# Optimization experiments

Hardware: AMD Instinct MI355X
Metric: run time of the kernel (lower is better)

Reference implementation:

```python
import jax, jax.numpy as jnp
import numpy as np

B, LQ, LK = 4, 2048, 2048
DIM = 1024          # intermediate_dim
H, D = 16, 64       # num_heads, head_dim
AD = H * D          # attn_dim
SCALE = 1.0 / np.sqrt(D).astype(np.float32)


def setup_inputs() -> dict:
    key = jax.random.key(0)
    ks = jax.random.split(key, 12)
    init = lambda k, shape, fan_in: jax.random.normal(k, shape, jnp.float32) / np.sqrt(fan_in).astype(np.float32)
    return {
        "x": jax.random.normal(ks[0], (B, LQ, DIM), jnp.float32),
        "embeds": jax.random.normal(ks[1], (B, LK, DIM), jnp.float32),
        "Wq": init(ks[2], (DIM, AD), DIM), "bq": jnp.zeros((AD,), jnp.float32),
        "Wk": init(ks[3], (DIM, AD), DIM), "bk": jnp.zeros((AD,), jnp.float32),
        "Wv": init(ks[4], (DIM, AD), DIM), "bv": jnp.zeros((AD,), jnp.float32),
        "Wo": init(ks[5], (AD, DIM), AD), "bo": jnp.zeros((DIM,), jnp.float32),
    }


def reference(x, embeds, Wq, bq, Wk, bk, Wv, bv, Wo, bo):
    b, lq, _ = x.shape
    lk = embeds.shape[1]
    # separate QKV projections (cross-attention: K,V from embeds)
    q = (x @ Wq + bq).reshape(b, lq, H, D)
    k = (embeds @ Wk + bk).reshape(b, lk, H, D)
    v = (embeds @ Wv + bv).reshape(b, lk, H, D)
    # scaled dot-product attention; full [b,h,lq,lk] score matrix (as in source)
    scores = jnp.einsum("bqhd,bkhd->bhqk", q, k) * SCALE
    attn = jax.nn.softmax(scores, axis=-1)  # dropout is identity at eval
    ctx = jnp.einsum("bhqk,bkhd->bqhd", attn, v).reshape(b, lq, AD)
    return ctx @ Wo + bo
```

## Files before the change

kernel.cpp:

```cpp
#include <hip/hip_runtime.h>
#include <cstdint>
#include <cstddef>

#define NB   4
#define NLQ  2048
#define NLK  2048
#define NDIM 1024
#define NH   16
#define ND   64
#define NAD  1024

typedef __attribute__((ext_vector_type(8))) short bf16x8;
typedef __attribute__((ext_vector_type(4))) short sh4;
typedef __attribute__((ext_vector_type(4))) float f32x4;
typedef __attribute__((ext_vector_type(4))) int   i32x4;

static __device__ __forceinline__ short f2bf(float f) {
    unsigned u = __builtin_bit_cast(unsigned, f);
    u += 0x7fffu + ((u >> 16) & 1u);
    return (short)(u >> 16);
}

#define GLL16(GP, LP) __builtin_amdgcn_global_load_lds( \
    (const __attribute__((address_space(1))) void*)(GP), \
    (__attribute__((address_space(3))) void*)(LP), 16, 0, 0)

__global__ void cvt2(const float* __restrict__ x, const float* __restrict__ e,
                     short* __restrict__ xo, short* __restrict__ eo) {
    const float* in = blockIdx.y ? e : x;
    short* out = blockIdx.y ? eo : xo;
    int i = (blockIdx.x * blockDim.x + threadIdx.x) * 4;
    const float4 v = *(const float4*)(in + i);
    sh4 o;
    o.x = f2bf(v.x); o.y = f2bf(v.y); o.z = f2bf(v.z); o.w = f2bf(v.w);
    *(sh4*)(out + i) = o;
}

__global__ void wtrans4(const float* __restrict__ W0, const float* __restrict__ W1,
                        const float* __restrict__ W2, const float* __restrict__ W3,
                        short* __restrict__ T0, short* __restrict__ T1,
                        short* __restrict__ T2, short* __restrict__ T3) {
    __shared__ float t[32][33];
    const int z = blockIdx.z;
    const float* W = (z == 0) ? W0 : (z == 1) ? W1 : (z == 2) ? W2 : W3;
    short* Wt = (z == 0) ? T0 : (z == 1) ? T1 : (z == 2) ? T2 : T3;
    const int bx = blockIdx.x * 32;
    const int by = blockIdx.y * 32;
    const int tx = threadIdx.x & 31, ty = threadIdx.x >> 5;
    #pragma unroll
    for (int i = 0; i < 32; i += 8)
        t[ty + i][tx] = W[(size_t)(bx + ty + i) * 1024 + by + tx];
    __syncthreads();
    #pragma unroll
    for (int i = 0; i < 32; i += 8)
        Wt[(size_t)(by + ty + i) * 1024 + bx + tx] = f2bf(t[tx][ty + i]);
}


__global__ __launch_bounds__(256) void gemm_qkv(const short* __restrict__ Xb,
                                                const short* __restrict__ Eb,
                                                const short* __restrict__ Wqt,
                                                const short* __restrict__ Wkt,
                                                const short* __restrict__ Wvt,
                                                const float* __restrict__ bq,
                                                const float* __restrict__ bk,
                                                const float* __restrict__ bv,
                                                short* __restrict__ Qb,
                                                short* __restrict__ Kf,
                                                short* __restrict__ Vtb)
{
    const int N = 1024, K = 1024;
    __shared__ __align__(16) short As[128 * 64];
    __shared__ __align__(16) short Bs[128 * 64];
    const int z = blockIdx.z;
    const short* A    = (z == 0) ? Xb : Eb;
    const short* Wt   = (z == 0) ? Wqt : (z == 1) ? Wkt : Wvt;
    const float* bias = (z == 0) ? bq : (z == 1) ? bk : bv;
    const float scale = (z == 0) ? 0.18033688011112042f : 1.0f;

    const int tid = threadIdx.x, wave = tid >> 6, lane = tid & 63;
    const int quad = lane >> 4, col = lane & 15;
    const int m0 = blockIdx.x * 128, n0 = blockIdx.y * 128;
    const int wm = wave >> 1, wn = wave & 1;

    const f32x4 zero = {0.f, 0.f, 0.f, 0.f};
    f32x4 acc[4][4];
    #pragma unroll
    for (int i = 0; i < 4; ++i)
        #pragma unroll
        for (int j = 0; j < 4; ++j)
            acc[i][j] = zero;

    for (int kt = 0; kt < K / 64; ++kt) {
        __syncthreads();
        #pragma unroll
        for (int i = 0; i < 4; ++i) {
            const int f = (i * 4 + wave) * 512 + lane * 8;
            const int row = f >> 6, ch = (f >> 3) & 7;
            const int gcol = kt * 64 + ((ch ^ (row & 7)) * 8);
            GLL16(A  + (size_t)(m0 + row) * K + gcol, &As[f]);
            GLL16(Wt + (size_t)(n0 + row) * K + gcol, &Bs[f]);
        }
        __syncthreads();
        #pragma unroll
        for (int kk = 0; kk < 2; ++kk) {
            bf16x8 af[4], bfr[4];
            #pragma unroll
            for (int mt = 0; mt < 4; ++mt) {
                const int r = wm * 64 + mt * 16 + col;
                af[mt] = *(const bf16x8*)&As[r * 64 + (((kk * 4 + quad) ^ (r & 7)) * 8)];
            }
            #pragma unroll
            for (int nt = 0; nt < 4; ++nt) {
                const int r = wn * 64 + nt * 16 + col;
                bfr[nt] = *(const bf16x8*)&Bs[r * 64 + (((kk * 4 + quad) ^ (r & 7)) * 8)];
            }
            #pragma unroll
            for (int mt = 0; mt < 4; ++mt)
                #pragma unroll
                for (int nt = 0; nt < 4; ++nt)
                    acc[mt][nt] = __builtin_amdgcn_mfma_f32_16x16x32_bf16(af[mt], bfr[nt], acc[mt][nt], 0, 0, 0);
        }
    }

    if (z < 2) {
        short* outp = (z == 0) ? Qb : Kf;
        #pragma unroll
        for (int mt = 0; mt < 4; ++mt)
            #pragma unroll
            for (int nt = 0; nt < 4; ++nt) {
                const int n = n0 + wn * 64 + nt * 16 + col;
                const float bv_ = bias[n];
                #pragma unroll
                for (int r = 0; r < 4; ++r) {
                    const int m = m0 + wm * 64 + mt * 16 + quad * 4 + r;
                    outp[(size_t)m * N + n] = f2bf((acc[mt][nt][r] + bv_) * scale);
                }
            }
    } else {
        #pragma unroll
        for (int mt = 0; mt < 4; ++mt)
            #pragma unroll
            for (int nt = 0; nt < 4; ++nt) {
                const int n = n0 + wn * 64 + nt * 16 + col;
                const int hh = n >> 6, d = n & 63;
                const float bv_ = bias[n];
                const int mb = m0 + wm * 64 + mt * 16 + quad * 4;
                const int bb = mb >> 11, s = mb & 2047;
                sh4 o4;
                #pragma unroll
                for (int r = 0; r < 4; ++r)
                    o4[r] = f2bf(acc[mt][nt][r] + bv_);
                *(sh4*)&Vtb[((size_t)((bb * NH + hh) * 64 + d)) * NLK + s] = o4;
            }
    }
}

__global__ __launch_bounds__(256) void gemm_out(const short* __restrict__ A,
                                                const short* __restrict__ Wt,
                                                const float* __restrict__ bias,
                                                float* __restrict__ outp)
{
    const int N = 1024, K = 1024;
    __shared__ __align__(16) short As[128 * 64];
    __shared__ __align__(16) short Bs[128 * 64];
    const int tid = threadIdx.x, wave = tid >> 6, lane = tid & 63;
    const int quad = lane >> 4, col = lane & 15;
    const int m0 = blockIdx.x * 128, n0 = blockIdx.y * 128;
    const int wm = wave >> 1, wn = wave & 1;

    const f32x4 zero = {0.f, 0.f, 0.f, 0.f};
    f32x4 acc[4][4];
    #pragma unroll
    for (int i = 0; i < 4; ++i)
        #pragma unroll
        for (int j = 0; j < 4; ++j)
            acc[i][j] = zero;

    for (int kt = 0; kt < K / 64; ++kt) {
        __syncthreads();
        #pragma unroll
        for (int i = 0; i < 4; ++i) {
            const int f = (i * 4 + wave) * 512 + lane * 8;
            const int row = f >> 6, ch = (f >> 3) & 7;
            const int gcol = kt * 64 + ((ch ^ (row & 7)) * 8);
            GLL16(A  + (size_t)(m0 + row) * K + gcol, &As[f]);
            GLL16(Wt + (size_t)(n0 + row) * K + gcol, &Bs[f]);
        }
        __syncthreads();
        #pragma unroll
        for (int kk = 0; kk < 2; ++kk) {
            bf16x8 af[4], bfr[4];
            #pragma unroll
            for (int mt = 0; mt < 4; ++mt) {
                const int r = wm * 64 + mt * 16 + col;
                af[mt] = *(const bf16x8*)&As[r * 64 + (((kk * 4 + quad) ^ (r & 7)) * 8)];
            }
            #pragma unroll
            for (int nt = 0; nt < 4; ++nt) {
                const int r = wn * 64 + nt * 16 + col;
                bfr[nt] = *(const bf16x8*)&Bs[r * 64 + (((kk * 4 + quad) ^ (r & 7)) * 8)];
            }
            #pragma unroll
            for (int mt = 0; mt < 4; ++mt)
                #pragma unroll
                for (int nt = 0; nt < 4; ++nt)
                    acc[mt][nt] = __builtin_amdgcn_mfma_f32_16x16x32_bf16(af[mt], bfr[nt], acc[mt][nt], 0, 0, 0);
        }
    }

    #pragma unroll
    for (int mt = 0; mt < 4; ++mt)
        #pragma unroll
        for (int nt = 0; nt < 4; ++nt) {
            const int n = n0 + wn * 64 + nt * 16 + col;
            const float bv_ = bias[n];
            #pragma unroll
            for (int r = 0; r < 4; ++r) {
                const int m = m0 + wm * 64 + mt * 16 + quad * 4 + r;
                outp[(size_t)m * N + n] = acc[mt][nt][r] + bv_;
            }
        }
}

__global__ __launch_bounds__(256, 2) void attn_fused6(const short* __restrict__ Q,
                                                      const short* __restrict__ Kb,
                                                      const short* __restrict__ Vt,
                                                      short* __restrict__ ctx)
{
    __shared__ __align__(16) short Ks[64 * 64];
    __shared__ __align__(16) short Vs[64 * 64];
    const int tid = threadIdx.x, wave = tid >> 6, lane = tid & 63;
    const int quad = lane >> 4, col = lane & 15;
    const int h = blockIdx.y, b = blockIdx.z;
    const int q0 = blockIdx.x * 256 + wave * 64;

    bf16x8 aq[4][2];
    #pragma unroll
    for (int mt = 0; mt < 4; ++mt) {
        const short* qp = Q + (size_t)(b * NLQ + q0 + mt * 16 + col) * NAD + h * 64 + quad * 8;
        aq[mt][0] = *(const bf16x8*)qp;
        aq[mt][1] = *(const bf16x8*)(qp + 32);
    }

    bf16x8 vones;
    #pragma unroll
    for (int j = 0; j < 8; ++j) vones[j] = (short)0x3F80;

    const f32x4 zero = {0.f, 0.f, 0.f, 0.f};
    f32x4 O[4][4];
    f32x4 Ol[4];
    #pragma unroll
    for (int mt = 0; mt < 4; ++mt) {
        Ol[mt] = zero;
        #pragma unroll
        for (int db = 0; db < 4; ++db) O[db][mt] = zero;
    }

    const int srow = tid >> 3, schunk = tid & 7;
    const short* kbase = Kb + (size_t)b * NLK * NAD + h * 64 + schunk * 8;
    const short* vbase = Vt + (size_t)(b * NH + h) * 64 * NLK + schunk * 8;

    bf16x8 kv[2], vv[2];
    #pragma unroll
    for (int i = 0; i < 2; ++i) {
        const int row = i * 32 + srow;
        kv[i] = *(const bf16x8*)(kbase + (size_t)row * NAD);
        vv[i] = *(const bf16x8*)(vbase + (size_t)row * NLK);
    }

    for (int kt = 0; kt < NLK / 64; ++kt) {
        __syncthreads();
        #pragma unroll
        for (int i = 0; i < 2; ++i) {
            const int row = i * 32 + srow;
            const int c = (schunk ^ (row & 7)) * 8;
            *(bf16x8*)&Ks[row * 64 + c] = kv[i];
            *(bf16x8*)&Vs[row * 64 + c] = vv[i];
        }
        __syncthreads();

        const int nk = (kt + 1) & (NLK / 64 - 1);
        #pragma unroll
        for (int i = 0; i < 2; ++i) {
            const int row = i * 32 + srow;
            kv[i] = *(const bf16x8*)(kbase + (size_t)(nk * 64 + row) * NAD);
            vv[i] = *(const bf16x8*)(vbase + (size_t)row * NLK + nk * 64);
        }

        bf16x8 kf[2][4];
        #pragma unroll
        for (int kk = 0; kk < 2; ++kk)
            #pragma unroll
            for (int nt = 0; nt < 4; ++nt) {
                const int key = nt * 16 + col;
                kf[kk][nt] = *(const bf16x8*)&Ks[key * 64 + (((kk * 4 + quad) ^ (key & 7)) * 8)];
            }

        int pk[4][2][4];
        #pragma unroll
        for (int mt = 0; mt < 4; ++mt) {
            f32x4 st[4];
            #pragma unroll
            for (int nt = 0; nt < 4; ++nt) st[nt] = zero;
            #pragma unroll
            for (int kk = 0; kk < 2; ++kk)
                #pragma unroll
                for (int nt = 0; nt < 4; ++nt)
                    st[nt] = __builtin_amdgcn_mfma_f32_16x16x32_bf16(kf[kk][nt], aq[mt][kk], st[nt], 0, 0, 0);
            #pragma unroll
            for (int nt = 0; nt < 4; ++nt) {
                const unsigned u0 = __builtin_bit_cast(unsigned, __builtin_amdgcn_exp2f(st[nt][0]));
                const unsigned u1 = __builtin_bit_cast(unsigned, __builtin_amdgcn_exp2f(st[nt][1]));
                const unsigned u2 = __builtin_bit_cast(unsigned, __builtin_amdgcn_exp2f(st[nt][2]));
                const unsigned u3 = __builtin_bit_cast(unsigned, __builtin_amdgcn_exp2f(st[nt][3]));
                const int t = nt >> 1, odd = (nt & 1) * 2;
                pk[mt][t][odd + 0] = (int)__builtin_amdgcn_perm(u1, u0, 0x07060302u);
                pk[mt][t][odd + 1] = (int)__builtin_amdgcn_perm(u3, u2, 0x07060302u);
            }
            #pragma unroll
            for (int t = 0; t < 2; ++t) {
                const bf16x8 pb = __builtin_bit_cast(bf16x8,
                    i32x4{pk[mt][t][0], pk[mt][t][1], pk[mt][t][2], pk[mt][t][3]});
                Ol[mt] = __builtin_amdgcn_mfma_f32_16x16x32_bf16(vones, pb, Ol[mt], 0, 0, 0);
            }
        }

        #pragma unroll
        for (int t = 0; t < 2; ++t)
            #pragma unroll
            for (int db = 0; db < 4; ++db) {
                const int row = db * 16 + col;
                const int c0 = t * 32 + quad * 4;
                const int c1 = t * 32 + 16 + quad * 4;
                const sh4 lo = *(const sh4*)&Vs[row * 64 + (((c0 >> 3) ^ (row & 7)) * 8 + (c0 & 7))];
                const sh4 hi = *(const sh4*)&Vs[row * 64 + (((c1 >> 3) ^ (row & 7)) * 8 + (c1 & 7))];
                bf16x8 va;
                #pragma unroll
                for (int j = 0; j < 4; ++j) { va[j] = lo[j]; va[j + 4] = hi[j]; }
                #pragma unroll
                for (int mt = 0; mt < 4; ++mt) {
                    const bf16x8 pb = __builtin_bit_cast(bf16x8,
                        i32x4{pk[mt][t][0], pk[mt][t][1], pk[mt][t][2], pk[mt][t][3]});
                    O[db][mt] = __builtin_amdgcn_mfma_f32_16x16x32_bf16(va, pb, O[db][mt], 0, 0, 0);
                }
            }
    }

    #pragma unroll
    for (int mt = 0; mt < 4; ++mt) {
        const float linv = 1.0f / Ol[mt][0];
        #pragma unroll
        for (int db = 0; db < 4; ++db) {
            sh4 o4;
            #pragma unroll
            for (int r = 0; r < 4; ++r)
                o4[r] = f2bf(O[db][mt][r] * linv);
            short* cp = ctx + (size_t)(b * NLQ + q0 + mt * 16 + col) * NAD
                      + h * 64 + db * 16 + quad * 4;
            *(sh4*)cp = o4;
        }
    }
}

extern "C" void kernel_launch(void* const* d_in, const int* in_sizes, int n_in,
                              void* d_out, int out_size, void* d_ws, size_t ws_size,
                              hipStream_t stream)
{
    (void)in_sizes; (void)n_in; (void)out_size; (void)ws_size;
    const float* x  = (const float*)d_in[0];
    const float* e  = (const float*)d_in[1];
    const float* Wq = (const float*)d_in[2];
    const float* bq = (const float*)d_in[3];
    const float* Wk = (const float*)d_in[4];
    const float* bk = (const float*)d_in[5];
    const float* Wv = (const float*)d_in[6];
    const float* bv = (const float*)d_in[7];
    const float* Wo = (const float*)d_in[8];
    const float* bo = (const float*)d_in[9];
    float* out = (float*)d_out;

    const size_t MQ = (size_t)NB * NLQ;
    short* wsp = (short*)d_ws;
    short* Xb  = wsp;
    short* Eb  = Xb  + MQ * NDIM;
    short* Wqt = Eb  + MQ * NDIM;
    short* Wkt = Wqt + (size_t)NDIM * NAD;
    short* Wvt = Wkt + (size_t)NDIM * NAD;
    short* Wot = Wvt + (size_t)NDIM * NAD;
    short* Qb  = Wot + (size_t)NDIM * NAD;
    short* Kf  = Qb  + MQ * NAD;
    short* Vtb = Kf  + MQ * NAD;
    short* Cx  = Vtb + MQ * NAD;

    cvt2<<<dim3(8192, 2), 256, 0, stream>>>(x, e, Xb, Eb);
    wtrans4<<<dim3(32, 32, 4), 256, 0, stream>>>(Wq, Wk, Wv, Wo, Wqt, Wkt, Wvt, Wot);

    gemm_qkv<<<dim3(64, 8, 3), 256, 0, stream>>>(Xb, Eb, Wqt, Wkt, Wvt,
                                                 bq, bk, bv, Qb, Kf, Vtb);

    attn_fused6<<<dim3(NLQ / 256, NH, NB), 256, 0, stream>>>(Qb, Kf, Vtb, Cx);

    gemm_out<<<dim3(64, 8), 256, 0, stream>>>(Cx, Wot, bo, out);
}
```

Before: 299.6 us.

## Rewrite QKV GEMM with 256x256 tiles, double-buffered LDS and scheduled barriers

The QKV projection GEMM moves from 128x128 tiles on 256 threads with synchronous single-buffer loads to 256x256 tiles on 512 threads. Global-to-LDS loads are double-buffered, with explicit vmcnt waits, so loads overlap the MFMA work. Each wave loads its fragments into registers and then runs the MFMA burst at raised priority between explicit barriers. Larger tiles improve data reuse, but the grid shrinks to 384 blocks and the kernel uses 128KB of LDS, which limits occupancy.

```diff
diff --git a/kernel.cpp b/kernel.cpp
--- a/kernel.cpp
+++ b/kernel.cpp
@@ -24,6 +24,12 @@
 #define GLL16(GP, LP) __builtin_amdgcn_global_load_lds( \
     (const __attribute__((address_space(1))) void*)(GP), \
     (__attribute__((address_space(3))) void*)(LP), 16, 0, 0)
+
+#define SBAR do { __builtin_amdgcn_sched_barrier(0); asm volatile("" ::: "memory"); \
+                  __builtin_amdgcn_s_barrier(); \
+                  asm volatile("" ::: "memory"); __builtin_amdgcn_sched_barrier(0); } while (0)
+#define WAITVM(N) do { asm volatile("s_waitcnt vmcnt(" #N ")" ::: "memory"); \
+                       __builtin_amdgcn_sched_barrier(0); } while (0)
 
 __global__ void cvt2(const float* __restrict__ x, const float* __restrict__ e,
                      short* __restrict__ xo, short* __restrict__ eo) {
@@ -56,22 +62,20 @@
         Wt[(size_t)(by + ty + i) * 1024 + bx + tx] = f2bf(t[tx][ty + i]);
 }
 
-
-__global__ __launch_bounds__(256) void gemm_qkv(const short* __restrict__ Xb,
-                                                const short* __restrict__ Eb,
-                                                const short* __restrict__ Wqt,
-                                                const short* __restrict__ Wkt,
-                                                const short* __restrict__ Wvt,
-                                                const float* __restrict__ bq,
-                                                const float* __restrict__ bk,
-                                                const float* __restrict__ bv,
-                                                short* __restrict__ Qb,
-                                                short* __restrict__ Kf,
-                                                short* __restrict__ Vtb)
+__global__ __launch_bounds__(512, 2) void gemm_qkv2(const short* __restrict__ Xb,
+                                                    const short* __restrict__ Eb,
+                                                    const short* __restrict__ Wqt,
+                                                    const short* __restrict__ Wkt,
+                                                    const short* __restrict__ Wvt,
+                                                    const float* __restrict__ bq,
+                                                    const float* __restrict__ bk,
+                                                    const float* __restrict__ bv,
+                                                    short* __restrict__ Qb,
+                                                    short* __restrict__ Kf,
+                                                    short* __restrict__ Vtb)
 {
-    const int N = 1024, K = 1024;
-    __shared__ __align__(16) short As[128 * 64];
-    __shared__ __align__(16) short Bs[128 * 64];
+    const int NT = 16;
+    __shared__ __align__(16) short lds[2][2 * 256 * 64];
     const int z = blockIdx.z;
     const short* A    = (z == 0) ? Xb : Eb;
     const short* Wt   = (z == 0) ? Wqt : (z == 1) ? Wkt : Wvt;
@@ -80,79 +84,114 @@
 
     const int tid = threadIdx.x, wave = tid >> 6, lane = tid & 63;
     const int quad = lane >> 4, col = lane & 15;
-    const int m0 = blockIdx.x * 128, n0 = blockIdx.y * 128;
-    const int wm = wave >> 1, wn = wave & 1;
+    const int m0 = blockIdx.x * 256, n0 = blockIdx.y * 256;
+    const int wm = wave >> 2, wn = wave & 3;
 
     const f32x4 zero = {0.f, 0.f, 0.f, 0.f};
-    f32x4 acc[4][4];
-    #pragma unroll
-    for (int i = 0; i < 4; ++i)
+    f32x4 acc[8][4];
+    #pragma unroll
+    for (int i = 0; i < 8; ++i)
         #pragma unroll
         for (int j = 0; j < 4; ++j)
             acc[i][j] = zero;
 
-    for (int kt = 0; kt < K / 64; ++kt) {
-        __syncthreads();
+    auto STAGE = [&](short* buf, int t) {
         #pragma unroll
         for (int i = 0; i < 4; ++i) {
-            const int f = (i * 4 + wave) * 512 + lane * 8;
-            const int row = f >> 6, ch = (f >> 3) & 7;
-            const int gcol = kt * 64 + ((ch ^ (row & 7)) * 8);
-            GLL16(A  + (size_t)(m0 + row) * K + gcol, &As[f]);
-            GLL16(Wt + (size_t)(n0 + row) * K + gcol, &Bs[f]);
-        }
-        __syncthreads();
-        #pragma unroll
-        for (int kk = 0; kk < 2; ++kk) {
-            bf16x8 af[4], bfr[4];
-            #pragma unroll
-            for (int mt = 0; mt < 4; ++mt) {
-                const int r = wm * 64 + mt * 16 + col;
-                af[mt] = *(const bf16x8*)&As[r * 64 + (((kk * 4 + quad) ^ (r & 7)) * 8)];
-            }
-            #pragma unroll
-            for (int nt = 0; nt < 4; ++nt) {
-                const int r = wn * 64 + nt * 16 + col;
-                bfr[nt] = *(const bf16x8*)&Bs[r * 64 + (((kk * 4 + quad) ^ (r & 7)) * 8)];
-            }
-            #pragma unroll
-            for (int mt = 0; mt < 4; ++mt)
-                #pragma unroll
-                for (int nt = 0; nt < 4; ++nt)
-                    acc[mt][nt] = __builtin_amdgcn_mfma_f32_16x16x32_bf16(af[mt], bfr[nt], acc[mt][nt], 0, 0, 0);
-        }
+            const int f = (i * 8 + wave) * 64 + lane;
+            const int row = f >> 3, ch = f & 7;
+            const int gcol = t * 64 + ((ch ^ (row & 7)) * 8);
+            GLL16(A  + (size_t)(m0 + row) * 1024 + gcol, buf + f * 8);
+            GLL16(Wt + (size_t)(n0 + row) * 1024 + gcol, buf + 256 * 64 + f * 8);
+        }
+    };
+
+    auto COMPUTE = [&](const short* Abuf, const short* Bbuf) {
+        #pragma unroll
+        for (int qm = 0; qm < 2; ++qm)
+            #pragma unroll
+            for (int qn = 0; qn < 2; ++qn) {
+                bf16x8 af[2][4], bfr[2][2];
+                #pragma unroll
+                for (int kk = 0; kk < 2; ++kk) {
+                    #pragma unroll
+                    for (int mt = 0; mt < 4; ++mt) {
+                        const int r = wm * 128 + qm * 64 + mt * 16 + col;
+                        af[kk][mt] = *(const bf16x8*)&Abuf[r * 64 + (((kk * 4 + quad) ^ (r & 7)) * 8)];
+                    }
+                    #pragma unroll
+                    for (int nt = 0; nt < 2; ++nt) {
+                        const int r = wn * 64 + qn * 32 + nt * 16 + col;
+                        bfr[kk][nt] = *(const bf16x8*)&Bbuf[r * 64 + (((kk * 4 + quad) ^ (r & 7)) * 8)];
+                    }
+                }
+                SBAR;
+                __builtin_amdgcn_s_setprio(1);
+                #pragma unroll
+                for (int kk = 0; kk < 2; ++kk)
+                    #pragma unroll
+                    for (int mt = 0; mt < 4; ++mt)
+                        #pragma unroll
+                        for (int nt = 0; nt < 2; ++nt)
+                            acc[qm * 4 + mt][qn * 2 + nt] =
+                                __builtin_amdgcn_mfma_f32_16x16x32_bf16(af[kk][mt], bfr[kk][nt],
+                                                                        acc[qm * 4 + mt][qn * 2 + nt], 0, 0, 0);
+                __builtin_amdgcn_s_setprio(0);
+                SBAR;
+            }
+    };
+
+    short* L0 = &lds[0][0];
+    short* L1 = &lds[1][0];
+
+    STAGE(L0, 0);
+    STAGE(L1, 1);
+    WAITVM(8);
+    SBAR;
+
+    for (int t2 = 0; t2 < NT; t2 += 2) {
+        COMPUTE(L0, L0 + 256 * 64);
+        SBAR;
+        if (t2 + 2 < NT) { STAGE(L0, t2 + 2); WAITVM(8); }
+        else             { WAITVM(0); }
+        SBAR;
+        COMPUTE(L1, L1 + 256 * 64);
+        SBAR;
+        if (t2 + 3 < NT) { STAGE(L1, t2 + 3); WAITVM(8); }
+        SBAR;
     }
 
     if (z < 2) {
         short* outp = (z == 0) ? Qb : Kf;
         #pragma unroll
-        for (int mt = 0; mt < 4; ++mt)
+        for (int mt = 0; mt < 8; ++mt) {
+            const int mbase = m0 + wm * 128 + (mt >> 2) * 64 + (mt & 3) * 16 + quad * 4;
             #pragma unroll
             for (int nt = 0; nt < 4; ++nt) {
-                const int n = n0 + wn * 64 + nt * 16 + col;
+                const int n = n0 + wn * 64 + (nt >> 1) * 32 + (nt & 1) * 16 + col;
                 const float bv_ = bias[n];
                 #pragma unroll
-                for (int r = 0; r < 4; ++r) {
-                    const int m = m0 + wm * 64 + mt * 16 + quad * 4 + r;
-                    outp[(size_t)m * N + n] = f2bf((acc[mt][nt][r] + bv_) * scale);
-                }
-            }
+                for (int r = 0; r < 4; ++r)
+                    outp[(size_t)(mbase + r) * 1024 + n] = f2bf((acc[mt][nt][r] + bv_) * scale);
+            }
+        }
     } else {
         #pragma unroll
-        for (int mt = 0; mt < 4; ++mt)
+        for (int mt = 0; mt < 8; ++mt) {
+            const int mb = m0 + wm * 128 + (mt >> 2) * 64 + (mt & 3) * 16 + quad * 4;
+            const int bb = mb >> 11, s = mb & 2047;
             #pragma unroll
             for (int nt = 0; nt < 4; ++nt) {
-                const int n = n0 + wn * 64 + nt * 16 + col;
+                const int n = n0 + wn * 64 + (nt >> 1) * 32 + (nt & 1) * 16 + col;
                 const int hh = n >> 6, d = n & 63;
                 const float bv_ = bias[n];
-                const int mb = m0 + wm * 64 + mt * 16 + quad * 4;
-                const int bb = mb >> 11, s = mb & 2047;
                 sh4 o4;
                 #pragma unroll
                 for (int r = 0; r < 4; ++r)
                     o4[r] = f2bf(acc[mt][nt][r] + bv_);
                 *(sh4*)&Vtb[((size_t)((bb * NH + hh) * 64 + d)) * NLK + s] = o4;
             }
+        }
     }
 }
 
@@ -396,8 +435,8 @@
     cvt2<<<dim3(8192, 2), 256, 0, stream>>>(x, e, Xb, Eb);
     wtrans4<<<dim3(32, 32, 4), 256, 0, stream>>>(Wq, Wk, Wv, Wo, Wqt, Wkt, Wvt, Wot);
 
-    gemm_qkv<<<dim3(64, 8, 3), 256, 0, stream>>>(Xb, Eb, Wqt, Wkt, Wvt,
-                                                 bq, bk, bv, Qb, Kf, Vtb);
+    gemm_qkv2<<<dim3(32, 4, 3), 512, 0, stream>>>(Xb, Eb, Wqt, Wkt, Wvt,
+                                                  bq, bk, bv, Qb, Kf, Vtb);
 
     attn_fused6<<<dim3(NLQ / 256, NH, NB), 256, 0, stream>>>(Qb, Kf, Vtb, Cx);
 
```

Result: slower. 328.4 us (+9.6%).

## Double-buffer K/V LDS tiles with one barrier and remap blocks for L2 locality

Applied to the files above, without the earlier changes.

The attention kernel now keeps two LDS buffers for the K and V tiles. That removes one of the two __syncthreads per key tile, leaving a single lgkmcnt wait plus barrier after the stores. The grid is flattened to 1D and block indices are remapped so that consecutive blocks cover different (batch, head) pairs within a query tile, which changes how K/V reuse spreads across caches. LDS use doubles to 32KB per block, which may limit occupancy. The single-barrier scheme relies on the alternating buffers being safe against the next iteration's writes.

```diff
diff --git a/kernel.cpp b/kernel.cpp
--- a/kernel.cpp
+++ b/kernel.cpp
@@ -24,6 +24,13 @@
 #define GLL16(GP, LP) __builtin_amdgcn_global_load_lds( \
     (const __attribute__((address_space(1))) void*)(GP), \
     (__attribute__((address_space(3))) void*)(LP), 16, 0, 0)
+
+#define SYNC_LDS do { \
+    __builtin_amdgcn_sched_barrier(0); \
+    asm volatile("s_waitcnt lgkmcnt(0)" ::: "memory"); \
+    __builtin_amdgcn_s_barrier(); \
+    asm volatile("" ::: "memory"); \
+    __builtin_amdgcn_sched_barrier(0); } while (0)
 
 __global__ void cvt2(const float* __restrict__ x, const float* __restrict__ e,
                      short* __restrict__ xo, short* __restrict__ eo) {
@@ -223,17 +230,21 @@
         }
 }
 
-__global__ __launch_bounds__(256, 2) void attn_fused6(const short* __restrict__ Q,
+__global__ __launch_bounds__(256, 2) void attn_fused7(const short* __restrict__ Q,
                                                       const short* __restrict__ Kb,
                                                       const short* __restrict__ Vt,
                                                       short* __restrict__ ctx)
 {
-    __shared__ __align__(16) short Ks[64 * 64];
-    __shared__ __align__(16) short Vs[64 * 64];
+    __shared__ __align__(16) short Ks[2][64 * 64];
+    __shared__ __align__(16) short Vs[2][64 * 64];
     const int tid = threadIdx.x, wave = tid >> 6, lane = tid & 63;
     const int quad = lane >> 4, col = lane & 15;
-    const int h = blockIdx.y, b = blockIdx.z;
-    const int q0 = blockIdx.x * 256 + wave * 64;
+
+    const int p = blockIdx.x;
+    const int g = ((p >> 3) & 7) * 8 + (p & 7);
+    const int qt = p >> 6;
+    const int h = g & 15, b = g >> 4;
+    const int q0 = qt * 256 + wave * 64;
 
     bf16x8 aq[4][2];
     #pragma unroll
@@ -270,15 +281,15 @@
     }
 
     for (int kt = 0; kt < NLK / 64; ++kt) {
-        __syncthreads();
+        short* Kw = &Ks[kt & 1][0];
+        short* Vw = &Vs[kt & 1][0];
         #pragma unroll
         for (int i = 0; i < 2; ++i) {
             const int row = i * 32 + srow;
             const int c = (schunk ^ (row & 7)) * 8;
-            *(bf16x8*)&Ks[row * 64 + c] = kv[i];
-            *(bf16x8*)&Vs[row * 64 + c] = vv[i];
-        }
-        __syncthreads();
+            *(bf16x8*)&Kw[row * 64 + c] = kv[i];
+            *(bf16x8*)&Vw[row * 64 + c] = vv[i];
+        }
 
         const int nk = (kt + 1) & (NLK / 64 - 1);
         #pragma unroll
@@ -288,13 +299,15 @@
             vv[i] = *(const bf16x8*)(vbase + (size_t)row * NLK + nk * 64);
         }
 
+        SYNC_LDS;
+
         bf16x8 kf[2][4];
         #pragma unroll
         for (int kk = 0; kk < 2; ++kk)
             #pragma unroll
             for (int nt = 0; nt < 4; ++nt) {
                 const int key = nt * 16 + col;
-                kf[kk][nt] = *(const bf16x8*)&Ks[key * 64 + (((kk * 4 + quad) ^ (key & 7)) * 8)];
+                kf[kk][nt] = *(const bf16x8*)&Kw[key * 64 + (((kk * 4 + quad) ^ (key & 7)) * 8)];
             }
 
         int pk[4][2][4];
@@ -333,8 +346,8 @@
                 const int row = db * 16 + col;
                 const int c0 = t * 32 + quad * 4;
                 const int c1 = t * 32 + 16 + quad * 4;
-                const sh4 lo = *(const sh4*)&Vs[row * 64 + (((c0 >> 3) ^ (row & 7)) * 8 + (c0 & 7))];
-                const sh4 hi = *(const sh4*)&Vs[row * 64 + (((c1 >> 3) ^ (row & 7)) * 8 + (c1 & 7))];
+                const sh4 lo = *(const sh4*)&Vw[row * 64 + (((c0 >> 3) ^ (row & 7)) * 8 + (c0 & 7))];
+                const sh4 hi = *(const sh4*)&Vw[row * 64 + (((c1 >> 3) ^ (row & 7)) * 8 + (c1 & 7))];
                 bf16x8 va;
                 #pragma unroll
                 for (int j = 0; j < 4; ++j) { va[j] = lo[j]; va[j + 4] = hi[j]; }
@@ -399,7 +412,7 @@
     gemm_qkv<<<dim3(64, 8, 3), 256, 0, stream>>>(Xb, Eb, Wqt, Wkt, Wvt,
                                                  bq, bk, bv, Qb, Kf, Vtb);
 
-    attn_fused6<<<dim3(NLQ / 256, NH, NB), 256, 0, stream>>>(Qb, Kf, Vtb, Cx);
+    attn_fused7<<<dim3(NB * NH * (NLQ / 256)), 256, 0, stream>>>(Qb, Kf, Vtb, Cx);
 
     gemm_out<<<dim3(64, 8), 256, 0, stream>>>(Cx, Wot, bo, out);
 }
```

Result: faster. 292.4 us (-2.4%).
